# Performance work log

Hardware: AMD Instinct MI355X
Metric: run time of the kernel (lower is better)

The kernel has to match this reference:

```python
import jax, jax.numpy as jnp
import numpy as np
from jax import lax

DN = ("NCDHW", "OIDHW", "NCDHW")


def bn(x, g, b, eps=1e-5):
    # torch BatchNorm3d training-mode forward: biased batch stats over (N, *, spatial)
    axes = (0,) + tuple(range(2, x.ndim))
    m = x.mean(axes, keepdims=True)
    v = x.var(axes, keepdims=True)
    shp = (1, -1) + (1,) * (x.ndim - 2)
    return (x - m) * lax.rsqrt(v + eps) * g.reshape(shp) + b.reshape(shp)


def conv_bn_relu(x, w, g, b, stride=(1, 1, 1), pad=(1, 0, 0)):
    y = lax.conv_general_dilated(x, w, stride, [(p, p) for p in pad], dimension_numbers=DN)
    return jax.nn.relu(bn(y, g, b))


def pw_bn_relu(x, w, g, b):  # 1x1x1 conv (no bias) + BN + ReLU on (B,C,T,H,W)
    y = jnp.einsum('oi,bithw->bothw', w, x)
    return jax.nn.relu(bn(y, g, b))


def pam_enc(x, pe_w, pe_g, pe_b):
    b, c, t, h, w = x.shape
    xm = x.mean(axis=2)  # all adaptive pools have T_out = 1
    feats = []
    for i, s in enumerate((1, 2, 3, 6)):  # H,W chosen divisible by 1,2,3,6 -> exact block means
        p = xm.reshape(b, c, s, h // s, s, w // s).mean(axis=(3, 5))  # (B,C,s,s)
        f = jnp.einsum('oi,bihw->bohw', pe_w[i], p)
        f = jax.nn.relu(bn(f, pe_g[i], pe_b[i]))
        feats.append(f.reshape(b, c, s * s))
    return jnp.concatenate(feats, axis=2)  # (B, C, 1+4+9+36=50)


def pam_dec(x, y, wq, bq, wk, bk, wv, bv, scale):
    # x: (B,C,T,H,W), y: (B,K,C)
    b, c, t, h, w = x.shape
    n = t * h * w
    q = jnp.einsum('oi,bithw->bothw', wq, x) + bq.reshape(1, -1, 1, 1, 1)
    q = q.reshape(b, c // 4, n).transpose(0, 2, 1)            # (B,N,C/4)
    k = y @ wk.T + bk                                         # (B,K,C/4)
    attn = jax.nn.softmax(jnp.einsum('bnd,bkd->bnk', q, k), axis=-1)
    v = y @ wv.T + bv                                         # (B,K,C)
    out = jnp.einsum('bkc,bnk->bcn', v, attn).reshape(b, c, t, h, w)
    return scale * out + x


def cam_dec(x, y, scale):
    b, c, t, h, w = x.shape
    xf = x.reshape(b, c, -1)
    yf = y.reshape(b, y.shape[1], -1)
    energy = jnp.einsum('bcn,bkn->bck', xf, yf)               # (B,C,K)
    attn = jax.nn.softmax(energy.max(-1, keepdims=True) - energy, axis=-1)
    out = jnp.einsum('bck,bkn->bcn', attn, yf).reshape(b, c, t, h, w)
    return x + scale * out


def tam_dec(x, y, scale):
    xp = x.transpose(0, 2, 1, 3, 4)  # (B,T,C,H,W)
    yp = y.transpose(0, 2, 1, 3, 4)
    b, t, c, h, w = xp.shape
    xf = xp.reshape(b, t, -1)
    yf = yp.reshape(b, t, -1)
    energy = jnp.einsum('bim,bjm->bij', xf, yf)               # (B,T,T)
    attn = jax.nn.softmax(energy.max(-1, keepdims=True) - energy, axis=-1)
    out = jnp.einsum('bij,bjm->bim', attn, yf).reshape(b, t, c, h, w)
    return (xp + scale * out).transpose(0, 2, 1, 3, 4)


def caf(x1, x2, w_conv1, g_conv1, b_conv1, w_conv2, g_conv2, b_conv2, w_tam, g_tam, b_tam, w_cat, g_cat, b_cat, pe_w, pe_g, pe_b, pd_wq, pd_bq, pd_wk, pd_bk, pd_wv, pd_bv, pd_scale, ce_w, ce_g, ce_b, cd_scale, te_w, te_g, te_b, td_scale):
    c1 = lambda z: conv_bn_relu(z, w_conv1, g_conv1, b_conv1)
    c2 = lambda z: conv_bn_relu(z, w_conv2, g_conv2, b_conv2)
    x1i = c1(x1)  # conv1(x1) is used by both PAM and CAM branches (identical in torch)
    x2i = c1(x2)
    # PAM branches
    x1_pa = c2(pam_dec(x1i, pam_enc(x1i, pe_w, pe_g, pe_b).transpose(0, 2, 1), pd_wq, pd_bq, pd_wk, pd_bk, pd_wv, pd_bv, pd_scale))
    x2_pa = c2(pam_dec(x2i, pam_enc(x2i, pe_w, pe_g, pe_b).transpose(0, 2, 1), pd_wq, pd_bq, pd_wk, pd_bk, pd_wv, pd_bv, pd_scale))
    # CAM branches
    x1_ca = c2(cam_dec(x1i, pw_bn_relu(x1i, ce_w, ce_g, ce_b), cd_scale))
    x2_ca = c2(cam_dec(x2i, pw_bn_relu(x2i, ce_w, ce_g, ce_b), cd_scale))
    # TAM branch over temporal concat (2T frames)
    xt1 = c1(jnp.concatenate([x1, x2], axis=2))
    xt2 = pw_bn_relu(xt1, te_w, te_g, te_b)
    x_ta = conv_bn_relu(tam_dec(xt1, xt2, td_scale), w_tam, g_tam, b_tam, stride=(2, 1, 1))
    out1 = conv_bn_relu(jnp.concatenate([x1_pa, x2_ca, x_ta], axis=1), w_cat, g_cat, b_cat)
    out2 = conv_bn_relu(jnp.concatenate([x2_pa, x1_ca, x_ta], axis=1), w_cat, g_cat, b_cat)
    return out1, out2


def setup_inputs() -> dict:
    key = jax.random.key(0)
    B, C, T, H, W = 4, 256, 16, 36, 36
    IC = C // 4
    ks = iter(jax.random.split(key, 24))
    rn = lambda shape, s=0.05: jax.random.normal(next(ks), shape, jnp.float32) * s
    ones = lambda n: jnp.ones((n,), jnp.float32)
    zeros = lambda n: jnp.zeros((n,), jnp.float32)
    return {
        "x1": rn((B, C, T, H, W), 1.0),
        "x2": rn((B, C, T, H, W), 1.0),
        "w_conv1": rn((IC, C, 3, 1, 1)), "g_conv1": ones(IC), "b_conv1": zeros(IC),
        "w_conv2": rn((IC, IC, 3, 1, 1)), "g_conv2": ones(IC), "b_conv2": zeros(IC),
        "w_tam": rn((IC, IC, 3, 1, 1)), "g_tam": ones(IC), "b_tam": zeros(IC),
        "w_cat": rn((C, 3 * IC, 3, 1, 1)), "g_cat": ones(C), "b_cat": zeros(C),
        "pe_w": rn((4, IC, IC)), "pe_g": jnp.ones((4, IC), jnp.float32), "pe_b": jnp.zeros((4, IC), jnp.float32),
        "pd_wq": rn((IC // 4, IC)), "pd_bq": zeros(IC // 4),
        "pd_wk": rn((IC // 4, IC)), "pd_bk": zeros(IC // 4),
        "pd_wv": rn((IC, IC)), "pd_bv": zeros(IC),
        "pd_scale": jnp.full((1,), 0.1, jnp.float32),
        "ce_w": rn((IC // 16, IC)), "ce_g": ones(IC // 16), "ce_b": zeros(IC // 16),
        "cd_scale": jnp.full((1,), 0.1, jnp.float32),
        "te_w": rn((IC, IC)), "te_g": ones(IC), "te_b": zeros(IC),
        "td_scale": jnp.full((1,), 0.1, jnp.float32),
    }


def reference(x1, x2, w_conv1, g_conv1, b_conv1, w_conv2, g_conv2, b_conv2, w_tam, g_tam, b_tam, w_cat, g_cat, b_cat, pe_w, pe_g, pe_b, pd_wq, pd_bq, pd_wk, pd_bk, pd_wv, pd_bv, pd_scale, ce_w, ce_g, ce_b, cd_scale, te_w, te_g, te_b, td_scale):
    return caf(x1, x2, w_conv1, g_conv1, b_conv1, w_conv2, g_conv2, b_conv2, w_tam, g_tam, b_tam, w_cat, g_cat, b_cat, pe_w, pe_g, pe_b, pd_wq, pd_bq, pd_wk, pd_bk, pd_wv, pd_bv, pd_scale, ce_w, ce_g, ce_b, cd_scale, te_w, te_g, te_b, td_scale)
```

## Files before the change

kernel.cpp:

```cpp
#include <hip/hip_runtime.h>

#define HW 1296
#define Tt 16
#define T2 32
#define Nn 20736
#define N2 41472
#define TAPAD 72

typedef short bf16x8 __attribute__((ext_vector_type(8)));
typedef float f32x4 __attribute__((ext_vector_type(4)));

__device__ inline unsigned short f2b(float f){
  union { float f; unsigned u; } v; v.f = f;
  unsigned r = v.u + 0x7FFF + ((v.u >> 16) & 1);
  return (unsigned short)(r >> 16);
}
__device__ inline float b2f(unsigned short u){
  union { unsigned u; float f; } v; v.u = ((unsigned)u) << 16; return v.f;
}
__device__ inline float b2f_lo(unsigned u){
  union { unsigned u; float f; } v; v.u = u << 16; return v.f;
}
__device__ inline float b2f_hi(unsigned u){
  union { unsigned u; float f; } v; v.u = u & 0xffff0000u; return v.f;
}

__device__ __forceinline__ void pack_pairs(const float* a, unsigned* vals){
  #pragma unroll
  for (int i = 0; i < 32; ++i)
    vals[i] = (unsigned)f2b(a[2*i]) | ((unsigned)f2b(a[2*i+1]) << 16);
}

__device__ __forceinline__ void staged_write(unsigned* lds, int tid, const unsigned* vals,
                                             uint4* o4, size_t R0, int rowu4, int cw,
                                             uint4* o4b){
  #pragma unroll
  for (int i = 0; i < 32; ++i) lds[tid*33 + i] = vals[i];
  __syncthreads();
  #pragma unroll
  for (int k = 0; k < 8; ++k){
    int j = k*256 + tid;
    int nn = j >> 3, w = j & 7;
    int base = nn*33 + w*4;
    uint4 v;
    v.x = lds[base]; v.y = lds[base+1]; v.z = lds[base+2]; v.w = lds[base+3];
    size_t oidx = (R0 + (size_t)nn)*(size_t)rowu4 + cw + w;
    o4[oidx] = v;
    if (o4b) o4b[oidx] = v;
  }
  __syncthreads();
}


__global__ void k_zero(float* p, int n){
  int i = blockIdx.x*blockDim.x + threadIdx.x;
  if (i < n) p[i] = 0.f;
}

__device__ __forceinline__ void wpack_one(int e, const float* w, unsigned short* wp,
                                          int Cout, int Cin, int KT){
  int Kt32 = (Cin*KT) >> 5;
  int j    = e & 7;
  int lane = (e >> 3) & 63;
  int rest = e >> 9;
  int ks   = rest % Kt32;
  int mt   = rest / Kt32;
  int m  = mt*16 + (lane & 15);
  int k  = ks*32 + (lane >> 4)*8 + j;
  int dt = k / Cin, ci = k - dt*Cin;
  wp[e] = f2b(w[((size_t)m*Cin + ci)*KT + dt]);
}

__global__ void k_wprep(const float* w1, const float* w2, const float* wt,
                        const float* wc, const float* wte, const float* wce,
                        unsigned short* Wp1, unsigned short* Wp2, unsigned short* Wpt,
                        unsigned short* Wpc, unsigned short* Wpte, float* wTce){
  int idx = blockIdx.x*256 + threadIdx.x;
  if (idx < 49152){ wpack_one(idx, w1, Wp1, 64, 256, 3); return; }
  idx -= 49152;
  if (idx < 12288){ wpack_one(idx, w2, Wp2, 64, 64, 3); return; }
  idx -= 12288;
  if (idx < 12288){ wpack_one(idx, wt, Wpt, 64, 64, 3); return; }
  idx -= 12288;
  if (idx < 147456){ wpack_one(idx, wc, Wpc, 256, 192, 3); return; }
  idx -= 147456;
  if (idx < 4096){ wpack_one(idx, wte, Wpte, 64, 64, 1); return; }
  idx -= 4096;
  if (idx < 256){
    int o = idx / 64, i = idx % 64;
    wTce[i*4 + o] = wce[idx];
  }
}

__global__ void k_convT(const float* __restrict__ x1, const float* __restrict__ x2,
                        unsigned short* __restrict__ Pb){
  __shared__ unsigned lds[8448];
  int tid = threadIdx.x, z = blockIdx.z;
  int b = z & 3;
  const float* x = (z < 4) ? x1 : x2;
  int p0 = (z < 4) ? 0 : 16;
  int n0 = blockIdx.x*256, n = n0 + tid;
  const float* xb = x + (size_t)b*256*Nn + n;
  size_t R0 = (size_t)(b*32 + p0)*1296 + n0;
  uint4* o4 = (uint4*)Pb;
  for (int c0 = 0; c0 < 256; c0 += 64){
    float a[64];
    #pragma unroll
    for (int c = 0; c < 64; ++c) a[c] = xb[(size_t)(c0 + c)*Nn];
    unsigned vals[32];
    pack_pairs(a, vals);
    staged_write(lds, tid, vals, o4, R0, 32, c0 >> 3, nullptr);
  }
}

__launch_bounds__(256)
__global__ void k_mfconv(const unsigned short* __restrict__ P, const unsigned short* __restrict__ Wp,
                         float* __restrict__ out, int Cin, int Cout, int Mz,
                         int Tout, int stride, int KT, int pad, int p0, int plo, int phi, int PT,
                         float* __restrict__ sums, int obf)
{
  __shared__ float sred[2][4][4][16];
  int bz = blockIdx.z; int b = bz / Mz; int mz = bz - b*Mz;
  int lane = threadIdx.x & 63;
  int wave = threadIdx.x >> 6;
  int tile = blockIdx.x*4 + wave;
  bool valid = (tile < 27);
  int t = blockIdx.y;
  int col = lane & 15, grp = lane >> 4;
  int Kt32 = (KT*Cin) >> 5;
  f32x4 acc[4][3];
  #pragma unroll
  for (int i = 0; i < 4; ++i)
    #pragma unroll
    for (int j = 0; j < 3; ++j) acc[i][j] = (f32x4){0.f, 0.f, 0.f, 0.f};
  if (valid){
    int hw0 = tile*48 + col;
    const unsigned short* wbase = Wp + ((size_t)(mz*4)*Kt32)*512 + lane*8;
    for (int dt = 0; dt < KT; ++dt){
      int p = t*stride + dt - pad + p0;
      if (p < plo || p >= phi) continue;
      const unsigned short* Pp = P + ((size_t)(b*PT + p)*1296 + hw0)*Cin + grp*8;
      int nCk = Cin >> 5;
      int ksg = (dt*Cin) >> 5;
      for (int kc = 0; kc < nCk; ++kc){
        bf16x8 bf0 = *(const bf16x8*)(Pp + (size_t)0*Cin  + kc*32);
        bf16x8 bf1 = *(const bf16x8*)(Pp + (size_t)16*Cin + kc*32);
        bf16x8 bf2 = *(const bf16x8*)(Pp + (size_t)32*Cin + kc*32);
        #pragma unroll
        for (int mf = 0; mf < 4; ++mf){
          bf16x8 af = *(const bf16x8*)(wbase + ((size_t)mf*Kt32 + ksg + kc)*512);
          acc[mf][0] = __builtin_amdgcn_mfma_f32_16x16x32_bf16(af, bf0, acc[mf][0], 0, 0, 0);
          acc[mf][1] = __builtin_amdgcn_mfma_f32_16x16x32_bf16(af, bf1, acc[mf][1], 0, 0, 0);
          acc[mf][2] = __builtin_amdgcn_mfma_f32_16x16x32_bf16(af, bf2, acc[mf][2], 0, 0, 0);
        }
      }
    }
    size_t cs = (size_t)Tout*1296;
    size_t obase = ((size_t)(b*Cout + mz*64 + grp*4))*cs + (size_t)t*1296;
    if (obf){
      unsigned short* o16 = (unsigned short*)out;
      #pragma unroll
      for (int mf = 0; mf < 4; ++mf)
        #pragma unroll
        for (int f = 0; f < 3; ++f){
          int hw = tile*48 + f*16 + col;
          #pragma unroll
          for (int r = 0; r < 4; ++r)
            o16[obase + (size_t)(mf*16 + r)*cs + hw] = f2b(acc[mf][f][r]);
        }
    } else {
      #pragma unroll
      for (int mf = 0; mf < 4; ++mf)
        #pragma unroll
        for (int f = 0; f < 3; ++f){
          int hw = tile*48 + f*16 + col;
          #pragma unroll
          for (int r = 0; r < 4; ++r)
            out[obase + (size_t)(mf*16 + r)*cs + hw] = acc[mf][f][r];
        }
    }
  }
  float s[16], q[16];
  #pragma unroll
  for (int mf = 0; mf < 4; ++mf)
    #pragma unroll
    for (int r = 0; r < 4; ++r){
      float v0 = acc[mf][0][r], v1 = acc[mf][1][r], v2 = acc[mf][2][r];
      s[mf*4+r] = v0 + v1 + v2;
      q[mf*4+r] = v0*v0 + v1*v1 + v2*v2;
    }
  #pragma unroll
  for (int m = 1; m <= 8; m <<= 1){
    #pragma unroll
    for (int j = 0; j < 16; ++j){
      s[j] += __shfl_xor(s[j], m);
      q[j] += __shfl_xor(q[j], m);
    }
  }
  if (col == 0){
    #pragma unroll
    for (int j = 0; j < 16; ++j){
      sred[0][wave][grp][j] = s[j];
      sred[1][wave][grp][j] = q[j];
    }
  }
  __syncthreads();
  int tid = threadIdx.x;
  if (tid < 128){
    int stat = tid >> 6, ch = tid & 63;
    int rr = ch & 3, gg = (ch >> 2) & 3, mm = ch >> 4;
    int j = mm*4 + rr;
    float v = sred[stat][0][gg][j] + sred[stat][1][gg][j]
            + sred[stat][2][gg][j] + sred[stat][3][gg][j];
    atomicAdd(&sums[stat*Cout + mz*64 + ch], v);
  }
}

__global__ void k_tconv(const float* __restrict__ xA,
                        const float* __restrict__ wT,
                        float* __restrict__ out,
                        float* __restrict__ sums)
{
  __shared__ float r1[4][64], r2[4][64];
  int b  = blockIdx.z;
  int o  = threadIdx.x;
  int ty = threadIdx.y;
  int t  = blockIdx.y;
  int hw4 = blockIdx.x*64 + ty;
  bool valid = (hw4 < 324);
  float4 acc = make_float4(0.f,0.f,0.f,0.f);
  if (valid){
    const float4* xr = (const float4*)xA + ((size_t)b*64*16 + t)*324 + hw4;
    const float* wp  = wT + o;
    size_t xstep = (size_t)16*324;
    for (int i = 0; i < 64; ++i){
      float4 xv = *xr;
      float  wv = *wp;
      acc.x = fmaf(wv, xv.x, acc.x);
      acc.y = fmaf(wv, xv.y, acc.y);
      acc.z = fmaf(wv, xv.z, acc.z);
      acc.w = fmaf(wv, xv.w, acc.w);
      xr += xstep; wp += 4;
    }
    float4* op = (float4*)out + ((size_t)(b*4 + o)*16 + t)*324 + hw4;
    *op = acc;
  }
  r1[o][ty] = acc.x + acc.y + acc.z + acc.w;
  r2[o][ty] = acc.x*acc.x + acc.y*acc.y + acc.z*acc.z + acc.w*acc.w;
  __syncthreads();
  int tid = threadIdx.y*4 + threadIdx.x;
  for (int k = 32; k > 0; k >>= 1){
    if (ty < k){
      r1[o][ty] += r1[o][ty+k];
      r2[o][ty] += r2[o][ty+k];
    }
    __syncthreads();
  }
  if (tid < 4) atomicAdd(&sums[tid],     r1[tid][0]);
  else if (tid < 8) atomicAdd(&sums[tid], r2[tid-4][0]);
}


__global__ void k_planestats(const float* __restrict__ A, const float* __restrict__ B,
                             float* __restrict__ s22, float* __restrict__ s23){
  int which = blockIdx.z, c = blockIdx.y, tid = threadIdx.x;
  const float* src = which ? B : A;
  int toff = which ? 0 : 15;
  float* dst = which ? s23 : s22;
  float s = 0.f, q = 0.f;
  for (int idx = tid; idx < 4*1296; idx += 256){
    int b = idx / 1296, hw = idx - b*1296;
    float v = src[(((size_t)b*64 + c)*16 + toff)*1296 + hw];
    s += v; q += v*v;
  }
  __shared__ float r1[256], r2[256];
  r1[tid] = s; r2[tid] = q; __syncthreads();
  for (int k = 128; k > 0; k >>= 1){
    if (tid < k){ r1[tid] += r1[tid+k]; r2[tid] += r2[tid+k]; }
    __syncthreads();
  }
  if (tid == 0){ dst[c] = r1[0]; dst[64 + c] = r2[0]; }
}

__global__ void k_combine(float* stats){
  int i = threadIdx.x;
  if (i < 128)
    stats[2*512 + i] = stats[0*512 + i] + stats[1*512 + i]
                     - stats[22*512 + i] - stats[23*512 + i] + stats[21*512 + i];
}

__global__ void k_bnrelu_out(const unsigned short* __restrict__ xbf,
                             const float* __restrict__ sums, const float* __restrict__ g,
                             const float* __restrict__ bet, float invc,
                             float* __restrict__ out)
{
  int c = blockIdx.y, b = blockIdx.z;
  int n8 = blockIdx.x*256 + threadIdx.x;
  if (n8 >= 2592) return;
  float m  = sums[c]*invc;
  float v  = fmaxf(sums[256+c]*invc - m*m, 0.f);
  float sc = g[c]*rsqrtf(v + 1e-5f);
  float bb = bet[c] - m*sc;
  size_t base = ((size_t)(b*256 + c))*Nn + (size_t)n8*8;
  uint4 u = *(const uint4*)(xbf + base);
  float4 o0, o1;
  o0.x = fmaxf(fmaf(b2f_lo(u.x), sc, bb), 0.f);
  o0.y = fmaxf(fmaf(b2f_hi(u.x), sc, bb), 0.f);
  o0.z = fmaxf(fmaf(b2f_lo(u.y), sc, bb), 0.f);
  o0.w = fmaxf(fmaf(b2f_hi(u.y), sc, bb), 0.f);
  o1.x = fmaxf(fmaf(b2f_lo(u.z), sc, bb), 0.f);
  o1.y = fmaxf(fmaf(b2f_hi(u.z), sc, bb), 0.f);
  o1.z = fmaxf(fmaf(b2f_lo(u.w), sc, bb), 0.f);
  o1.w = fmaxf(fmaf(b2f_hi(u.w), sc, bb), 0.f);
  *(float4*)(out + base) = o0;
  *(float4*)(out + base + 4) = o1;
}

__global__ void k_bnrelu_mean(float* __restrict__ x, const float* __restrict__ sums,
                              const float* __restrict__ g, const float* __restrict__ bet,
                              float invc, float* __restrict__ p6)
{
  __shared__ float p6loc[36];
  int tid = threadIdx.x;
  if (tid < 36) p6loc[tid] = 0.f;
  __syncthreads();
  int hw = blockIdx.x*256 + tid;
  int c = blockIdx.y, b = blockIdx.z;
  if (hw < 1296){
    float m  = sums[c]*invc;
    float v  = fmaxf(sums[64+c]*invc - m*m, 0.f);
    float sc = g[c]*rsqrtf(v + 1e-5f);
    float bb = bet[c] - m*sc;
    float* xb = x + ((size_t)(b*64 + c)*16)*1296 + hw;
    float s = 0.f;
    #pragma unroll
    for (int t = 0; t < 16; ++t){
      float val = fmaxf(fmaf(xb[(size_t)t*1296], sc, bb), 0.f);
      xb[(size_t)t*1296] = val;
      s += val;
    }
    int h = hw / 36, w = hw - h*36;
    atomicAdd(&p6loc[(h/6)*6 + (w/6)], s*(1.f/16.f));
  }
  __syncthreads();
  if (tid < 36) atomicAdd(&p6[((size_t)(b*64 + c))*36 + tid], p6loc[tid]);
}

__global__ void k_bnT(const void* __restrict__ xraw, const float* __restrict__ sums,
                      const float* __restrict__ g, const float* __restrict__ bet, float invc,
                      unsigned short* __restrict__ P1, unsigned short* __restrict__ P2,
                      int L, int outC, int coff, int xbf)
{
  __shared__ unsigned lds[8448];
  int tid = threadIdx.x, b = blockIdx.z;
  int n0 = blockIdx.x*256, n = n0 + tid;
  float a[64];
  if (xbf){
    const unsigned short* xb = (const unsigned short*)xraw + (size_t)b*64*L + n;
    #pragma unroll
    for (int c = 0; c < 64; ++c){
      float m  = sums[c]*invc;
      float vv = fmaxf(sums[64+c]*invc - m*m, 0.f);
      float sc = g[c]*rsqrtf(vv + 1e-5f);
      float bb = bet[c] - m*sc;
      a[c] = fmaxf(fmaf(b2f(xb[(size_t)c*L]), sc, bb), 0.f);
    }
  } else {
    const float* xb = (const float*)xraw + (size_t)b*64*L + n;
    #pragma unroll
    for (int c = 0; c < 64; ++c){
      float m  = sums[c]*invc;
      float vv = fmaxf(sums[64+c]*invc - m*m, 0.f);
      float sc = g[c]*rsqrtf(vv + 1e-5f);
      float bb = bet[c] - m*sc;
      a[c] = fmaxf(fmaf(xb[(size_t)c*L], sc, bb), 0.f);
    }
  }
  unsigned vals[32];
  pack_pairs(a, vals);
  staged_write(lds, tid, vals, (uint4*)P1, (size_t)b*L + n0, outC >> 3, coff >> 3,
               P2 ? (uint4*)P2 : nullptr);
}

__global__ void k_bnT_cc(const float* __restrict__ A, const float* __restrict__ M,
                         const float* __restrict__ B, const float* __restrict__ sums,
                         const float* __restrict__ g, const float* __restrict__ bet,
                         float invc, unsigned short* __restrict__ P1)
{
  __shared__ unsigned lds[8448];
  int tid = threadIdx.x, b = blockIdx.z;
  int n0 = blockIdx.x*256, n = n0 + tid;
  int t = n / 1296, hw = n - t*1296;
  const float* src; size_t cstride;
  if (t < 15){ src = A + ((size_t)(b*64)*16 + t)*1296 + hw; cstride = (size_t)16*1296; }
  else if (t < 17){ src = M + ((size_t)(b*64)*2 + (t-15))*1296 + hw; cstride = (size_t)2*1296; }
  else { src = B + ((size_t)(b*64)*16 + (t-16))*1296 + hw; cstride = (size_t)16*1296; }
  float a[64];
  #pragma unroll
  for (int c = 0; c < 64; ++c){
    float m  = sums[c]*invc;
    float vv = fmaxf(sums[64+c]*invc - m*m, 0.f);
    float sc = g[c]*rsqrtf(vv + 1e-5f);
    float bb = bet[c] - m*sc;
    a[c] = fmaxf(fmaf(src[c*cstride], sc, bb), 0.f);
  }
  unsigned vals[32];
  pack_pairs(a, vals);
  staged_write(lds, tid, vals, (uint4*)P1, (size_t)b*N2 + n0, 8, 0, nullptr);
}


__global__ void k_pamenc1(const float* __restrict__ p6, const float* __restrict__ pe_w,
                          float* __restrict__ pf, float* __restrict__ sl){
  __shared__ float psh[64];
  int cell = blockIdx.x, b = blockIdx.z;
  int o = threadIdx.x;
  int s, off;
  if (cell < 1){ s=1; off=0; } else if (cell < 5){ s=2; off=1; }
  else if (cell < 14){ s=3; off=5; } else { s=6; off=14; }
  int local = cell - off, ph = local/s, pw = local%s;
  int bs = 6/s;
  const float* pp = p6 + ((size_t)(b*64 + o))*36;
  float sum = 0.f;
  for (int i = 0; i < bs; ++i)
    for (int j = 0; j < bs; ++j)
      sum += pp[(ph*bs + i)*6 + (pw*bs + j)];
  psh[o] = sum * ((float)(s*s) * (1.f/1296.f));
  __syncthreads();
  int grp = (cell < 1) ? 0 : (cell < 5) ? 1 : (cell < 14) ? 2 : 3;
  const float* w = pe_w + (size_t)grp*4096 + o*64;
  float acc = 0.f;
  #pragma unroll
  for (int i = 0; i < 64; ++i) acc = fmaf(w[i], psh[i], acc);
  pf[((size_t)b*64 + o)*50 + cell] = acc;
  atomicAdd(&sl[grp*128 + o], acc);
  atomicAdd(&sl[grp*128 + 64 + o], acc*acc);
}

__launch_bounds__(128)
__global__ void k_pamenc2(const float* __restrict__ pf, const float* __restrict__ sl,
                          const float* __restrict__ pe_g, const float* __restrict__ pe_b,
                          const float* __restrict__ wk, const float* __restrict__ bk,
                          const float* __restrict__ wv, const float* __restrict__ bv,
                          const float* __restrict__ wq, const float* __restrict__ bq,
                          float* __restrict__ vb, float* __restrict__ KW,
                          float* __restrict__ sb)
{
  __shared__ float yk[64];
  __shared__ float kbl[16];
  int k = blockIdx.x, b = blockIdx.z;
  int tid = threadIdx.x;
  int grp = (k < 1) ? 0 : (k < 5) ? 1 : (k < 14) ? 2 : 3;
  const float ss2[4] = {1.f, 4.f, 9.f, 36.f};
  if (tid < 64){
    float invc = 1.f/(4.f*ss2[grp]);
    float m = sl[grp*128 + tid]*invc;
    float var = fmaxf(sl[grp*128 + 64 + tid]*invc - m*m, 0.f);
    float sc = pe_g[grp*64 + tid]*rsqrtf(var + 1e-5f);
    float sh = pe_b[grp*64 + tid] - m*sc;
    yk[tid] = fmaxf(fmaf(pf[((size_t)b*64 + tid)*50 + k], sc, sh), 0.f);
  }
  __syncthreads();
  if (tid < 16){
    float s = bk[tid];
    #pragma unroll
    for (int c = 0; c < 64; ++c) s = fmaf(wk[tid*64 + c], yk[c], s);
    kbl[tid] = s;
  } else if (tid < 80){
    int c = tid - 16;
    float s = bv[c];
    #pragma unroll
    for (int i = 0; i < 64; ++i) s = fmaf(wv[c*64 + i], yk[i], s);
    vb[((size_t)b*50 + k)*64 + c] = s;
  }
  __syncthreads();
  if (tid < 64){
    float s = 0.f;
    #pragma unroll
    for (int o = 0; o < 16; ++o) s = fmaf(kbl[o], wq[o*64 + tid], s);
    KW[((size_t)b*50 + k)*64 + tid] = s;
  } else if (tid == 64){
    float s = 0.f;
    #pragma unroll
    for (int o = 0; o < 16; ++o) s = fmaf(kbl[o], bq[o], s);
    sb[(size_t)b*50 + k] = s;
  }
}

__launch_bounds__(256, 1)
__global__ void k_pamattn(const float* __restrict__ x, const float* __restrict__ KW,
                          const float* __restrict__ sbb, const float* __restrict__ vbuf,
                          const float* __restrict__ scp, unsigned short* __restrict__ Pg)
{
  __shared__ unsigned smem_u[8448];
  float* smem = (float*)smem_u;
  int b = blockIdx.z, tid = threadIdx.x;
  for (int i = tid; i < 3200; i += 256){
    smem[i]        = KW[(size_t)b*3200 + i];
    smem[3200 + i] = vbuf[(size_t)b*3200 + i];
  }
  if (tid < 50) smem[6400 + tid] = sbb[(size_t)b*50 + tid];
  __syncthreads();
  int n0 = blockIdx.x*256;
  int n = n0 + tid;
  const float* xb = x + (size_t)b*64*Nn + n;
  float xv[64];
  #pragma unroll
  for (int c = 0; c < 64; ++c) xv[c] = xb[(size_t)c*Nn];
  float s[50];
  const float4* kw4 = (const float4*)smem;
  #pragma unroll
  for (int k = 0; k < 50; ++k){
    float t = smem[6400 + k];
    #pragma unroll
    for (int c4 = 0; c4 < 16; ++c4){
      float4 kw = kw4[k*16 + c4];
      t = fmaf(xv[c4*4+0], kw.x, t);
      t = fmaf(xv[c4*4+1], kw.y, t);
      t = fmaf(xv[c4*4+2], kw.z, t);
      t = fmaf(xv[c4*4+3], kw.w, t);
    }
    s[k] = t;
  }
  float mx = -1e30f;
  #pragma unroll
  for (int k = 0; k < 50; ++k) mx = fmaxf(mx, s[k]);
  float sum = 0.f;
  #pragma unroll
  for (int k = 0; k < 50; ++k){ float p = __expf(s[k]-mx); s[k] = p; sum += p; }
  float sc = scp[0]/sum;
  const float4* vl4 = (const float4*)(smem + 3200);
  #pragma unroll
  for (int k = 0; k < 50; ++k){
    float pk = sc * s[k];
    #pragma unroll
    for (int c4 = 0; c4 < 16; ++c4){
      float4 v = vl4[k*16 + c4];
      xv[c4*4+0] = fmaf(pk, v.x, xv[c4*4+0]);
      xv[c4*4+1] = fmaf(pk, v.y, xv[c4*4+1]);
      xv[c4*4+2] = fmaf(pk, v.z, xv[c4*4+2]);
      xv[c4*4+3] = fmaf(pk, v.w, xv[c4*4+3]);
    }
  }
  __syncthreads();
  unsigned vals[32];
  pack_pairs(xv, vals);
  staged_write(smem_u, tid, vals, (uint4*)Pg, (size_t)b*Nn + n0, 8, 0, nullptr);
}


__global__ void k_camenergy2(const float* __restrict__ x, const float* __restrict__ yc,
                             const float* __restrict__ sums, const float* __restrict__ ce_g,
                             const float* __restrict__ ce_b, float invc,
                             float* __restrict__ e){
  __shared__ float yl[4][256];
  int b = blockIdx.z, tid = threadIdx.x;
  int n0 = blockIdx.x*256;
  #pragma unroll
  for (int k = 0; k < 4; ++k){
    float m  = sums[k]*invc;
    float vv = fmaxf(sums[4+k]*invc - m*m, 0.f);
    float sck = ce_g[k]*rsqrtf(vv + 1e-5f);
    float bbk = ce_b[k] - m*sck;
    float raw = yc[((size_t)b*4+k)*Nn + n0 + tid];
    yl[k][tid] = fmaxf(fmaf(raw, sck, bbk), 0.f);
  }
  __syncthreads();
  int c = tid & 63, ks = tid >> 6;
  const float* xr = x + (size_t)(b*64+c)*Nn + n0;
  const float* yr = yl[ks];
  float acc = 0.f;
  #pragma unroll 8
  for (int i = 0; i < 256; ++i) acc = fmaf(xr[i], yr[i], acc);
  atomicAdd(&e[((size_t)(b*64)+c)*4 + ks], acc);
}

__global__ void k_camapplyT(const float* __restrict__ x, const float* __restrict__ yc,
                            const float* __restrict__ sums, const float* __restrict__ ce_g,
                            const float* __restrict__ ce_b, float invc,
                            const float* __restrict__ e, const float* __restrict__ scp,
                            unsigned short* __restrict__ Pg){
  __shared__ float pw[64][4];
  __shared__ unsigned lds[8448];
  int tid = threadIdx.x;
  int b = blockIdx.z;
  if (tid < 64){
    const float* er = e + (size_t)(b*64+tid)*4;
    float e0=er[0], e1=er[1], e2=er[2], e3=er[3];
    float mx = fmaxf(fmaxf(e0,e1), fmaxf(e2,e3));
    float z0=mx-e0, z1=mx-e1, z2=mx-e2, z3=mx-e3;
    float zm = fmaxf(fmaxf(z0,z1), fmaxf(z2,z3));
    float p0=__expf(z0-zm), p1=__expf(z1-zm), p2=__expf(z2-zm), p3=__expf(z3-zm);
    float inv = 1.f/(p0+p1+p2+p3);
    pw[tid][0]=p0*inv; pw[tid][1]=p1*inv; pw[tid][2]=p2*inv; pw[tid][3]=p3*inv;
  }
  __syncthreads();
  int n0 = blockIdx.x*256;
  int n = n0 + tid;
  float yv[4];
  #pragma unroll
  for (int k = 0; k < 4; ++k){
    float m  = sums[k]*invc;
    float vv = fmaxf(sums[4+k]*invc - m*m, 0.f);
    float sck = ce_g[k]*rsqrtf(vv + 1e-5f);
    float bbk = ce_b[k] - m*sck;
    yv[k] = fmaxf(fmaf(yc[((size_t)b*4+k)*Nn + n], sck, bbk), 0.f);
  }
  float sc = scp[0];
  const float* xb = x + (size_t)b*64*Nn + n;
  float a[64];
  #pragma unroll
  for (int c = 0; c < 64; ++c){
    a[c] = fmaf(sc, pw[c][0]*yv[0] + pw[c][1]*yv[1] + pw[c][2]*yv[2] + pw[c][3]*yv[3],
                xb[(size_t)c*Nn]);
  }
  unsigned vals[32];
  pack_pairs(a, vals);
  staged_write(lds, tid, vals, (uint4*)Pg, (size_t)b*Nn + n0, 8, 0, nullptr);
}


__launch_bounds__(256)
__global__ void k_tamenergy_mf(const unsigned short* __restrict__ X,
                               const unsigned short* __restrict__ Y,
                               float* __restrict__ E){
  int b = blockIdx.z;
  int wave = threadIdx.x >> 6, lane = threadIdx.x & 63;
  int r = lane & 15, g = lane >> 4;
  const unsigned short* Xb = X + (size_t)b*32*82944;
  const unsigned short* Yb = Y + (size_t)b*32*82944;
  f32x4 a00 = (f32x4){0.f,0.f,0.f,0.f};
  f32x4 a01 = a00, a10 = a00, a11 = a00;
  int c0 = (blockIdx.x*4 + wave)*8;
  for (int cc = 0; cc < 8; ++cc){
    size_t k0 = (size_t)(c0 + cc)*32 + (size_t)g*8;
    bf16x8 x0 = *(const bf16x8*)(Xb + (size_t)r*82944 + k0);
    bf16x8 x1 = *(const bf16x8*)(Xb + (size_t)(r+16)*82944 + k0);
    bf16x8 y0 = *(const bf16x8*)(Yb + (size_t)r*82944 + k0);
    bf16x8 y1 = *(const bf16x8*)(Yb + (size_t)(r+16)*82944 + k0);
    a00 = __builtin_amdgcn_mfma_f32_16x16x32_bf16(x0, y0, a00, 0, 0, 0);
    a01 = __builtin_amdgcn_mfma_f32_16x16x32_bf16(x0, y1, a01, 0, 0, 0);
    a10 = __builtin_amdgcn_mfma_f32_16x16x32_bf16(x1, y0, a10, 0, 0, 0);
    a11 = __builtin_amdgcn_mfma_f32_16x16x32_bf16(x1, y1, a11, 0, 0, 0);
  }
  float* Eb = E + (size_t)b*1024;
  #pragma unroll
  for (int rr = 0; rr < 4; ++rr){
    int row = g*4 + rr;
    atomicAdd(&Eb[row*32 + r],           a00[rr]);
    atomicAdd(&Eb[row*32 + 16 + r],      a01[rr]);
    atomicAdd(&Eb[(row+16)*32 + r],      a10[rr]);
    atomicAdd(&Eb[(row+16)*32 + 16 + r], a11[rr]);
  }
}

__launch_bounds__(256)
__global__ void k_tamapply_mf(const unsigned short* __restrict__ Xbf,
                              const unsigned short* __restrict__ Ybf,
                              const float* __restrict__ e, const float* __restrict__ scp,
                              unsigned short* __restrict__ Pout){
  __shared__ unsigned short yl[32*8*TAPAD];
  __shared__ float al[1024];
  int b = blockIdx.z, tid = threadIdx.x;
  int hw0 = blockIdx.x*8;
  if (tid < 32){
    const float* er = e + (size_t)b*1024 + tid*32;
    float mx = -1e30f, mn = 1e30f;
    for (int j = 0; j < 32; ++j){ mx = fmaxf(mx, er[j]); mn = fminf(mn, er[j]); }
    float zmax = mx - mn;
    float sum = 0.f;
    for (int j = 0; j < 32; ++j){
      float p = __expf((mx - er[j]) - zmax);
      al[tid*32 + j] = p; sum += p;
    }
    float inv = 1.f/sum;
    for (int j = 0; j < 32; ++j) al[tid*32 + j] *= inv;
  }
  const uint4* src = (const uint4*)Ybf + (size_t)b*N2*8;
  #pragma unroll
  for (int it = 0; it < 8; ++it){
    int idx = it*256 + tid;
    int j = idx >> 6, rem = idx & 63, h = rem >> 3, w = rem & 7;
    uint4 v = src[(size_t)(j*1296 + hw0 + h)*8 + w];
    *(uint4*)&yl[(j*8+h)*TAPAD + w*8] = v;
  }
  __syncthreads();
  int t = tid >> 3, h = tid & 7;
  int n = t*1296 + hw0 + h;
  float sc = scp[0];
  const uint4* xr = (const uint4*)Xbf + ((size_t)b*N2 + n)*8;
  float acc[64];
  #pragma unroll
  for (int w = 0; w < 8; ++w){
    uint4 v = xr[w];
    acc[w*8+0] = b2f_lo(v.x); acc[w*8+1] = b2f_hi(v.x);
    acc[w*8+2] = b2f_lo(v.y); acc[w*8+3] = b2f_hi(v.y);
    acc[w*8+4] = b2f_lo(v.z); acc[w*8+5] = b2f_hi(v.z);
    acc[w*8+6] = b2f_lo(v.w); acc[w*8+7] = b2f_hi(v.w);
  }
  const float* ar = &al[t*32];
  for (int j = 0; j < 32; ++j){
    float aj = sc * ar[j];
    const uint4* yr = (const uint4*)&yl[(j*8+h)*TAPAD];
    #pragma unroll
    for (int w = 0; w < 8; ++w){
      uint4 v = yr[w];
      acc[w*8+0] = fmaf(aj, b2f_lo(v.x), acc[w*8+0]);
      acc[w*8+1] = fmaf(aj, b2f_hi(v.x), acc[w*8+1]);
      acc[w*8+2] = fmaf(aj, b2f_lo(v.y), acc[w*8+2]);
      acc[w*8+3] = fmaf(aj, b2f_hi(v.y), acc[w*8+3]);
      acc[w*8+4] = fmaf(aj, b2f_lo(v.z), acc[w*8+4]);
      acc[w*8+5] = fmaf(aj, b2f_hi(v.z), acc[w*8+5]);
      acc[w*8+6] = fmaf(aj, b2f_lo(v.w), acc[w*8+6]);
      acc[w*8+7] = fmaf(aj, b2f_hi(v.w), acc[w*8+7]);
    }
  }
  uint4* orow = (uint4*)Pout + ((size_t)b*N2 + n)*8;
  #pragma unroll
  for (int w = 0; w < 8; ++w){
    uint4 v;
    v.x = (unsigned)f2b(acc[w*8+0]) | ((unsigned)f2b(acc[w*8+1]) << 16);
    v.y = (unsigned)f2b(acc[w*8+2]) | ((unsigned)f2b(acc[w*8+3]) << 16);
    v.z = (unsigned)f2b(acc[w*8+4]) | ((unsigned)f2b(acc[w*8+5]) << 16);
    v.w = (unsigned)f2b(acc[w*8+6]) | ((unsigned)f2b(acc[w*8+7]) << 16);
    orow[w] = v;
  }
}


extern "C" void kernel_launch(void* const* d_in, const int* in_sizes, int n_in,
                              void* d_out, int out_size, void* d_ws, size_t ws_size,
                              hipStream_t stream) {
  const float* x1      = (const float*)d_in[0];
  const float* x2      = (const float*)d_in[1];
  const float* w_conv1 = (const float*)d_in[2];
  const float* g_conv1 = (const float*)d_in[3];
  const float* b_conv1 = (const float*)d_in[4];
  const float* w_conv2 = (const float*)d_in[5];
  const float* g_conv2 = (const float*)d_in[6];
  const float* b_conv2 = (const float*)d_in[7];
  const float* w_tam   = (const float*)d_in[8];
  const float* g_tam   = (const float*)d_in[9];
  const float* b_tam   = (const float*)d_in[10];
  const float* w_cat   = (const float*)d_in[11];
  const float* g_cat   = (const float*)d_in[12];
  const float* b_cat   = (const float*)d_in[13];
  const float* pe_w    = (const float*)d_in[14];
  const float* pe_g    = (const float*)d_in[15];
  const float* pe_b    = (const float*)d_in[16];
  const float* pd_wq   = (const float*)d_in[17];
  const float* pd_bq   = (const float*)d_in[18];
  const float* pd_wk   = (const float*)d_in[19];
  const float* pd_bk   = (const float*)d_in[20];
  const float* pd_wv   = (const float*)d_in[21];
  const float* pd_bv   = (const float*)d_in[22];
  const float* pd_scale= (const float*)d_in[23];
  const float* ce_w    = (const float*)d_in[24];
  const float* ce_g    = (const float*)d_in[25];
  const float* ce_b    = (const float*)d_in[26];
  const float* cd_scale= (const float*)d_in[27];
  const float* te_w    = (const float*)d_in[28];
  const float* te_g    = (const float*)d_in[29];
  const float* te_b    = (const float*)d_in[30];
  const float* td_scale= (const float*)d_in[31];

  float* ws = (float*)d_ws;
  size_t off = 0;
  auto alloc = [&](size_t n){ float* p = ws + off; off += (n + 3) & ~(size_t)3; return p; };
  float* stats = alloc(16384);
  float* e_tam = alloc(4096);
  float* e_cam = alloc(2048);
  float* p6a   = alloc(9216);
  float* p6b   = alloc(9216);
  float* wTce  = alloc(256);
  unsigned short* Wp1  = (unsigned short*)alloc(24576);
  unsigned short* Wp2  = (unsigned short*)alloc(6144);
  unsigned short* Wpt  = (unsigned short*)alloc(6144);
  unsigned short* Wpc  = (unsigned short*)alloc(73728);
  unsigned short* Wpte = (unsigned short*)alloc(2048);
  float* pfb   = alloc(12800);
  float* vb    = alloc(12800);
  float* KWb   = alloc(12800);
  float* sbb   = alloc(256);
  float* yc    = alloc(331776);
  float* Mb    = alloc(663552);
  float* A     = alloc(5308416);
  float* Bb    = alloc(5308416);
  float* PTEf  = alloc(5308416);
  float* COMB  = alloc(31850496);

  unsigned short* P0 = (unsigned short*)COMB;
  unsigned short* DdBF = (unsigned short*)COMB;
  unsigned short* Dbf  = (unsigned short*)(COMB + 10616832);
  unsigned short* PTAM = (unsigned short*)(COMB + 15925248);
  unsigned short* RrawBF = (unsigned short*)COMB;
  unsigned short* PCAT1 = (unsigned short*)(COMB + 5308416);
  unsigned short* PCAT2 = (unsigned short*)(COMB + 13271040);
  unsigned short* PG    = (unsigned short*)(COMB + 21233664);
  unsigned short* CATR  = (unsigned short*)(COMB + 21233664);
  unsigned short* PTE = (unsigned short*)PTEf;

  const float invc16 = 1.f/(4.f*20736.f);
  const float invc32 = 1.f/(4.f*41472.f);

  k_zero<<<dim3(160), 256, 0, stream>>>(stats, 40960);
  k_wprep<<<dim3(881), 256, 0, stream>>>(w_conv1, w_conv2, w_tam, w_cat, te_w, ce_w,
                                         Wp1, Wp2, Wpt, Wpc, Wpte, wTce);
  k_convT<<<dim3(81, 1, 8), 256, 0, stream>>>(x1, x2, P0);

  k_mfconv<<<dim3(7,16,4), 256, 0, stream>>>(P0, Wp1, A,  256, 64, 1, 16, 1, 3, 1, 0, 0, 16, 32, stats + 0*512, 0);
  k_mfconv<<<dim3(7,16,4), 256, 0, stream>>>(P0, Wp1, Bb, 256, 64, 1, 16, 1, 3, 1, 16, 16, 32, 32, stats + 1*512, 0);
  k_mfconv<<<dim3(7,2,4),  256, 0, stream>>>(P0, Wp1, Mb, 256, 64, 1, 2, 1, 3, 1, 15, 0, 32, 32, stats + 21*512, 0);
  k_planestats<<<dim3(1,64,2), 256, 0, stream>>>(A, Bb, stats + 22*512, stats + 23*512);
  k_combine<<<dim3(1), 128, 0, stream>>>(stats);
  k_bnT_cc<<<dim3(162,1,4), 256, 0, stream>>>(A, Mb, Bb, stats + 2*512,
                                              g_conv1, b_conv1, invc32, PTE);

  k_mfconv<<<dim3(7,32,4), 256, 0, stream>>>(PTE, Wpte, (float*)DdBF, 64, 64, 1, 32, 1, 1, 0, 0, 0, 32, 32, stats + 3*512, 1);
  k_bnT<<<dim3(162,1,4), 256, 0, stream>>>(DdBF, stats + 3*512, te_g, te_b, invc32,
                                           Dbf, nullptr, N2, 64, 0, 1);

  k_tamenergy_mf<<<dim3(81, 1, 4), 256, 0, stream>>>(PTE, Dbf, e_tam);
  k_tamapply_mf<<<dim3(162, 1, 4), 256, 0, stream>>>(PTE, Dbf, e_tam, td_scale, PTAM);
  k_mfconv<<<dim3(7,16,4), 256, 0, stream>>>(PTAM, Wpt, (float*)RrawBF, 64, 64, 1, 16, 2, 3, 1, 0, 0, 32, 32, stats + 4*512, 1);
  k_bnT<<<dim3(81,1,4), 256, 0, stream>>>(RrawBF, stats + 4*512, g_tam, b_tam, invc16,
                                          PCAT1, PCAT2, Nn, 192, 128, 1);

  auto pam = [&](float* xin, const float* p6, unsigned short* catp, int slot_pe, int slot_c2){
    k_pamenc1<<<dim3(50, 1, 4), 64, 0, stream>>>(p6, pe_w, pfb, stats + (size_t)slot_pe*512);
    k_pamenc2<<<dim3(50, 1, 4), 128, 0, stream>>>(pfb, stats + (size_t)slot_pe*512,
                                                  pe_g, pe_b, pd_wk, pd_bk, pd_wv, pd_bv,
                                                  pd_wq, pd_bq, vb, KWb, sbb);
    k_pamattn<<<dim3(81, 1, 4), 256, 0, stream>>>(xin, KWb, sbb, vb, pd_scale, PG);
    k_mfconv<<<dim3(7,16,4), 256, 0, stream>>>(PG, Wp2, (float*)RrawBF, 64, 64, 1, 16, 1, 3, 1, 0, 0, 16, 16, stats + (size_t)slot_c2*512, 1);
    k_bnT<<<dim3(81,1,4), 256, 0, stream>>>(RrawBF, stats + (size_t)slot_c2*512,
                                            g_conv2, b_conv2, invc16, catp, nullptr, Nn, 192, 0, 1);
  };
  auto cam = [&](const float* xin, unsigned short* catp, float* ecam,
                 int slot_ce, int slot_c2){
    float* sums_ce = stats + (size_t)slot_ce*512;
    k_tconv<<<dim3(6, 16, 4), dim3(4, 64), 0, stream>>>(xin, wTce, yc, sums_ce);
    k_camenergy2<<<dim3(81, 1, 4), 256, 0, stream>>>(xin, yc, sums_ce, ce_g, ce_b, invc16, ecam);
    k_camapplyT<<<dim3(81, 1, 4), 256, 0, stream>>>(xin, yc, sums_ce, ce_g, ce_b, invc16,
                                                    ecam, cd_scale, PG);
    k_mfconv<<<dim3(7,16,4), 256, 0, stream>>>(PG, Wp2, (float*)RrawBF, 64, 64, 1, 16, 1, 3, 1, 0, 0, 16, 16, stats + (size_t)slot_c2*512, 1);
    k_bnT<<<dim3(81,1,4), 256, 0, stream>>>(RrawBF, stats + (size_t)slot_c2*512,
                                            g_conv2, b_conv2, invc16, catp, nullptr, Nn, 192, 64, 1);
  };

  k_bnrelu_mean<<<dim3(6,64,4), 256, 0, stream>>>(A, stats + 0*512, g_conv1, b_conv1,
                                                  invc16, p6a);
  pam(A, p6a, PCAT1, 5, 13);
  cam(A, PCAT2, e_cam, 15, 17);
  k_bnrelu_mean<<<dim3(6,64,4), 256, 0, stream>>>(Bb, stats + 1*512, g_conv1, b_conv1,
                                                  invc16, p6b);
  pam(Bb, p6b, PCAT2, 9, 14);
  cam(Bb, PCAT1, e_cam + 1024, 16, 18);

  float* out1 = (float*)d_out;
  float* out2 = out1 + (size_t)4*256*Nn;
  k_mfconv<<<dim3(7,16,16), 256, 0, stream>>>(PCAT1, Wpc, (float*)CATR, 192, 256, 4, 16, 1, 3, 1, 0, 0, 16, 16, stats + 19*512, 1);
  k_bnrelu_out<<<dim3(11, 256, 4), 256, 0, stream>>>(CATR, stats + 19*512, g_cat, b_cat,
                                                     invc16, out1);
  k_mfconv<<<dim3(7,16,16), 256, 0, stream>>>(PCAT2, Wpc, (float*)CATR, 192, 256, 4, 16, 1, 3, 1, 0, 0, 16, 16, stats + 20*512, 1);
  k_bnrelu_out<<<dim3(11, 256, 4), 256, 0, stream>>>(CATR, stats + 20*512, g_cat, b_cat,
                                                     invc16, out2);
}
```

Baseline: 923.5 us.

## Add wider-tile cat conv kernel and merge both BN-ReLU output passes

Adds a specialized MFMA conv kernel for the final concat convolution in which each block computes two 64-channel output groups, so every loaded activation fragment is reused across twice as many output channels. This halves the grid in z and cuts redundant activation loads. The two final BN+ReLU output launches are merged into one by writing the second conv result to a separate buffer (reusing A). The new kernel holds twice the accumulators, which raises register pressure and may lower occupancy.

```diff
diff --git a/kernel.cpp b/kernel.cpp
--- a/kernel.cpp
+++ b/kernel.cpp
@@ -213,6 +213,108 @@
     float v = sred[stat][0][gg][j] + sred[stat][1][gg][j]
             + sred[stat][2][gg][j] + sred[stat][3][gg][j];
     atomicAdd(&sums[stat*Cout + mz*64 + ch], v);
+  }
+}
+
+__launch_bounds__(256)
+__global__ void k_mfconv2(const unsigned short* __restrict__ P, const unsigned short* __restrict__ Wp,
+                          unsigned short* __restrict__ out, int Cin, int Tout,
+                          int KT, int pad, int PT, float* __restrict__ sums)
+{
+  __shared__ float sred[2][4][4][16];
+  const int Cout = 256;
+  int bz = blockIdx.z; int b = bz >> 1; int mz0 = (bz & 1)*2;
+  int lane = threadIdx.x & 63;
+  int wave = threadIdx.x >> 6;
+  int tile = blockIdx.x*4 + wave;
+  bool valid = (tile < 27);
+  int t = blockIdx.y;
+  int col = lane & 15, grp = lane >> 4;
+  int Kt32 = (KT*Cin) >> 5;
+  f32x4 acc[8][3];
+  #pragma unroll
+  for (int i = 0; i < 8; ++i)
+    #pragma unroll
+    for (int j = 0; j < 3; ++j) acc[i][j] = (f32x4){0.f, 0.f, 0.f, 0.f};
+  if (valid){
+    int hw0 = tile*48 + col;
+    const unsigned short* wb0 = Wp + ((size_t)(mz0*4)*Kt32)*512 + lane*8;
+    const unsigned short* wb1 = Wp + ((size_t)((mz0+1)*4)*Kt32)*512 + lane*8;
+    for (int dt = 0; dt < KT; ++dt){
+      int p = t + dt - pad;
+      if (p < 0 || p >= Tout) continue;
+      const unsigned short* Pp = P + ((size_t)(b*PT + p)*1296 + hw0)*Cin + grp*8;
+      int nCk = Cin >> 5;
+      int ksg = (dt*Cin) >> 5;
+      for (int kc = 0; kc < nCk; ++kc){
+        bf16x8 bf0 = *(const bf16x8*)(Pp + (size_t)0*Cin  + kc*32);
+        bf16x8 bf1 = *(const bf16x8*)(Pp + (size_t)16*Cin + kc*32);
+        bf16x8 bf2 = *(const bf16x8*)(Pp + (size_t)32*Cin + kc*32);
+        #pragma unroll
+        for (int mf = 0; mf < 4; ++mf){
+          bf16x8 af0 = *(const bf16x8*)(wb0 + ((size_t)mf*Kt32 + ksg + kc)*512);
+          acc[mf][0] = __builtin_amdgcn_mfma_f32_16x16x32_bf16(af0, bf0, acc[mf][0], 0, 0, 0);
+          acc[mf][1] = __builtin_amdgcn_mfma_f32_16x16x32_bf16(af0, bf1, acc[mf][1], 0, 0, 0);
+          acc[mf][2] = __builtin_amdgcn_mfma_f32_16x16x32_bf16(af0, bf2, acc[mf][2], 0, 0, 0);
+          bf16x8 af1 = *(const bf16x8*)(wb1 + ((size_t)mf*Kt32 + ksg + kc)*512);
+          acc[4+mf][0] = __builtin_amdgcn_mfma_f32_16x16x32_bf16(af1, bf0, acc[4+mf][0], 0, 0, 0);
+          acc[4+mf][1] = __builtin_amdgcn_mfma_f32_16x16x32_bf16(af1, bf1, acc[4+mf][1], 0, 0, 0);
+          acc[4+mf][2] = __builtin_amdgcn_mfma_f32_16x16x32_bf16(af1, bf2, acc[4+mf][2], 0, 0, 0);
+        }
+      }
+    }
+    size_t cs = (size_t)Tout*1296;
+    #pragma unroll
+    for (int mzi = 0; mzi < 2; ++mzi){
+      size_t obase = ((size_t)(b*Cout + (mz0+mzi)*64 + grp*4))*cs + (size_t)t*1296;
+      #pragma unroll
+      for (int mf = 0; mf < 4; ++mf)
+        #pragma unroll
+        for (int f = 0; f < 3; ++f){
+          int hw = tile*48 + f*16 + col;
+          #pragma unroll
+          for (int r = 0; r < 4; ++r)
+            out[obase + (size_t)(mf*16 + r)*cs + hw] = f2b(acc[mzi*4+mf][f][r]);
+        }
+    }
+  }
+  int tid = threadIdx.x;
+  #pragma unroll
+  for (int mzi = 0; mzi < 2; ++mzi){
+    if (mzi) __syncthreads();
+    float s[16], q[16];
+    #pragma unroll
+    for (int mf = 0; mf < 4; ++mf)
+      #pragma unroll
+      for (int r = 0; r < 4; ++r){
+        float v0 = acc[mzi*4+mf][0][r], v1 = acc[mzi*4+mf][1][r], v2 = acc[mzi*4+mf][2][r];
+        s[mf*4+r] = v0 + v1 + v2;
+        q[mf*4+r] = v0*v0 + v1*v1 + v2*v2;
+      }
+    #pragma unroll
+    for (int m = 1; m <= 8; m <<= 1){
+      #pragma unroll
+      for (int j = 0; j < 16; ++j){
+        s[j] += __shfl_xor(s[j], m);
+        q[j] += __shfl_xor(q[j], m);
+      }
+    }
+    if (col == 0){
+      #pragma unroll
+      for (int j = 0; j < 16; ++j){
+        sred[0][wave][grp][j] = s[j];
+        sred[1][wave][grp][j] = q[j];
+      }
+    }
+    __syncthreads();
+    if (tid < 128){
+      int stat = tid >> 6, ch = tid & 63;
+      int rr = ch & 3, gg = (ch >> 2) & 3, mm = ch >> 4;
+      int j = mm*4 + rr;
+      float v = sred[stat][0][gg][j] + sred[stat][1][gg][j]
+              + sred[stat][2][gg][j] + sred[stat][3][gg][j];
+      atomicAdd(&sums[stat*Cout + (mz0+mzi)*64 + ch], v);
+    }
   }
 }
 
@@ -289,12 +391,19 @@
                      - stats[22*512 + i] - stats[23*512 + i] + stats[21*512 + i];
 }
 
-__global__ void k_bnrelu_out(const unsigned short* __restrict__ xbf,
-                             const float* __restrict__ sums, const float* __restrict__ g,
+__global__ void k_bnrelu_out(const unsigned short* __restrict__ x1bf,
+                             const unsigned short* __restrict__ x2bf,
+                             const float* __restrict__ stats19,
+                             const float* __restrict__ g,
                              const float* __restrict__ bet, float invc,
                              float* __restrict__ out)
 {
-  int c = blockIdx.y, b = blockIdx.z;
+  int z = blockIdx.z;
+  int b = z & 3, which = z >> 2;
+  const unsigned short* xbf = which ? x2bf : x1bf;
+  const float* sums = stats19 + (size_t)which*512;
+  float* op = out + (size_t)which*4*256*Nn;
+  int c = blockIdx.y;
   int n8 = blockIdx.x*256 + threadIdx.x;
   if (n8 >= 2592) return;
   float m  = sums[c]*invc;
@@ -312,8 +421,8 @@
   o1.y = fmaxf(fmaf(b2f_hi(u.z), sc, bb), 0.f);
   o1.z = fmaxf(fmaf(b2f_lo(u.w), sc, bb), 0.f);
   o1.w = fmaxf(fmaf(b2f_hi(u.w), sc, bb), 0.f);
-  *(float4*)(out + base) = o0;
-  *(float4*)(out + base + 4) = o1;
+  *(float4*)(op + base) = o0;
+  *(float4*)(op + base + 4) = o1;
 }
 
 __global__ void k_bnrelu_mean(float* __restrict__ x, const float* __restrict__ sums,
@@ -797,7 +906,8 @@
   unsigned short* PCAT1 = (unsigned short*)(COMB + 5308416);
   unsigned short* PCAT2 = (unsigned short*)(COMB + 13271040);
   unsigned short* PG    = (unsigned short*)(COMB + 21233664);
-  unsigned short* CATR  = (unsigned short*)(COMB + 21233664);
+  unsigned short* CATR1 = (unsigned short*)(COMB + 21233664);
+  unsigned short* CATR2 = (unsigned short*)A;
   unsigned short* PTE = (unsigned short*)PTEf;
 
   const float invc16 = 1.f/(4.f*20736.f);
@@ -857,12 +967,8 @@
   pam(Bb, p6b, PCAT2, 9, 14);
   cam(Bb, PCAT1, e_cam + 1024, 16, 18);
 
-  float* out1 = (float*)d_out;
-  float* out2 = out1 + (size_t)4*256*Nn;
-  k_mfconv<<<dim3(7,16,16), 256, 0, stream>>>(PCAT1, Wpc, (float*)CATR, 192, 256, 4, 16, 1, 3, 1, 0, 0, 16, 16, stats + 19*512, 1);
-  k_bnrelu_out<<<dim3(11, 256, 4), 256, 0, stream>>>(CATR, stats + 19*512, g_cat, b_cat,
-                                                     invc16, out1);
-  k_mfconv<<<dim3(7,16,16), 256, 0, stream>>>(PCAT2, Wpc, (float*)CATR, 192, 256, 4, 16, 1, 3, 1, 0, 0, 16, 16, stats + 20*512, 1);
-  k_bnrelu_out<<<dim3(11, 256, 4), 256, 0, stream>>>(CATR, stats + 20*512, g_cat, b_cat,
-                                                     invc16, out2);
-}
+  k_mfconv2<<<dim3(7,16,8), 256, 0, stream>>>(PCAT1, Wpc, CATR1, 192, 16, 3, 1, 16, stats + 19*512);
+  k_mfconv2<<<dim3(7,16,8), 256, 0, stream>>>(PCAT2, Wpc, CATR2, 192, 16, 3, 1, 16, stats + 20*512);
+  k_bnrelu_out<<<dim3(11, 256, 8), 256, 0, stream>>>(CATR1, CATR2, stats + 19*512,
+                                                     g_cat, b_cat, invc16, (float*)d_out);
+}
```

Result: slower. 1.038 ms (+12.4%).
